# Kernel optimization log

Measured on AMD Instinct MI355X. Metric: run time of the kernel, lower is better.

The kernel has to match this reference:

```python
import jax, jax.numpy as jnp
import numpy as np

S, B, D, NH = 4096, 4, 1024, 16


def _unitnorm(v):
    # v / ||v||_2 along last dim (matches torch.norm(v, dim=-1))
    return v / jnp.linalg.norm(v, axis=-1, keepdims=True)


def setup_inputs() -> dict:
    key = jax.random.key(0)
    ks = jax.random.split(key, 9)
    scale = 1.0 / np.sqrt(D)
    inp = {
        "h": jax.random.normal(ks[0], (S, B, D), dtype=jnp.float32),
        "Wq_w": jax.random.normal(ks[1], (D, D), dtype=jnp.float32) * scale,
        "Wq_b": jax.random.normal(ks[2], (D,), dtype=jnp.float32) * scale,
        "Wk_w": jax.random.normal(ks[3], (D, D), dtype=jnp.float32) * scale,
        "Wk_b": jax.random.normal(ks[4], (D,), dtype=jnp.float32) * scale,
        "Wv_w": jax.random.normal(ks[5], (D, D), dtype=jnp.float32) * scale,
        "Wv_b": jax.random.normal(ks[6], (D,), dtype=jnp.float32) * scale,
        "Wo_w": jax.random.normal(ks[7], (D, D), dtype=jnp.float32) * scale,
        "Wo_b": jax.random.normal(ks[8], (D,), dtype=jnp.float32) * scale,
        "nhead": NH,
    }
    return inp


def reference(h, Wq_w, Wq_b, Wk_w, Wk_b, Wv_w, Wv_b, Wo_w, Wo_b, nhead):
    s, b, d = h.shape
    dh = d // nhead

    def proj(W, bias):
        # torch nn.Linear: x @ W.T + b, then split heads -> [S,B,NH,dh]
        return (h @ W.T + bias).reshape(s, b, nhead, dh)

    k = jax.nn.elu(_unitnorm(proj(Wk_w, Wk_b)))  # unitelu
    v = proj(Wv_w, Wv_b)
    q = _unitnorm(proj(Wq_w, Wq_b))  # sigma = unitnorm (default)

    # Linear-attention state: sum of outer products over the whole sequence
    A = jnp.einsum('sbnq,sbnv->bnvq', k, v)  # [B,NH,dh,dh]
    out = jnp.einsum('sbnq,bnvq->sbnv', q, A).reshape(s, b, d)
    out = out @ Wo_w.T + Wo_b
    return out, k, q
```

## Files before the change

### kernel.cpp

```cpp
#include <hip/hip_runtime.h>
#include <hip/hip_bf16.h>
#include <math.h>

#define S_LEN 4096
#define B_SZ  4
#define D_DIM 1024
#define NHEAD 16
#define R_ROWS (S_LEN * B_SZ)

#define AS1 __attribute__((address_space(1)))
#define AS3 __attribute__((address_space(3)))

typedef __bf16 bf16_t;
typedef __attribute__((ext_vector_type(8))) __bf16 bf16x8;
typedef __attribute__((ext_vector_type(4))) __bf16 bf16x4;
typedef __attribute__((ext_vector_type(4))) float  f32x4;

#define MFMA16 __builtin_amdgcn_mfma_f32_16x16x32_bf16

__device__ __forceinline__ void gload16(const bf16_t* g, bf16_t* l) {
  __builtin_amdgcn_global_load_lds((const AS1 unsigned int*)g,
                                   (AS3 unsigned int*)l, 16, 0, 0);
}

#define BAR asm volatile("s_barrier" ::: "memory")
#define LGKM0 do { asm volatile("s_waitcnt lgkmcnt(0)" ::: "memory"); \
                   __builtin_amdgcn_sched_barrier(0); } while (0)

#define RD_A(dst, ap, mlo) \
  _Pragma("unroll") for (int mm = 0; mm < 4; ++mm) \
    _Pragma("unroll") for (int kx = 0; kx < 2; ++kx) \
      dst[mm][kx] = *(const bf16x8*)&ap[offA[(mlo) + mm][kx]];
#define RD_B(dst, bp, nlo) \
  _Pragma("unroll") for (int nn = 0; nn < 2; ++nn) \
    _Pragma("unroll") for (int kx = 0; kx < 2; ++kx) \
      dst[nn][kx] = *(const bf16x8*)&bp[offB[(nlo) + nn][kx]];
#define QUAD(mb, nb, AF, BF) \
  do { __builtin_amdgcn_s_setprio(1); \
  _Pragma("unroll") for (int kx = 0; kx < 2; ++kx) \
    _Pragma("unroll") for (int mm = 0; mm < 4; ++mm) \
      _Pragma("unroll") for (int nn = 0; nn < 2; ++nn) \
        acc[(mb)+mm][(nb)+nn] = MFMA16(AF[mm][kx], BF[nn][kx], acc[(mb)+mm][(nb)+nn], 0, 0, 0); \
  __builtin_amdgcn_s_setprio(0); } while (0)

__global__ void k_cvt(const float* __restrict__ src, bf16_t* __restrict__ dst, int n) {
  int i = (blockIdx.x * 256 + threadIdx.x) * 4;
  if (i >= n) return;
  f32x4 v = *(const f32x4*)(src + i);
  bf16x4 o;
  o[0] = (bf16_t)v[0]; o[1] = (bf16_t)v[1]; o[2] = (bf16_t)v[2]; o[3] = (bf16_t)v[3];
  *(bf16x4*)(dst + i) = o;
}
__global__ void k_cvtw(const float* __restrict__ q, const float* __restrict__ k,
                       const float* __restrict__ v, const float* __restrict__ o,
                       bf16_t* __restrict__ dst) {
  const int sec = blockIdx.x >> 10;
  const int i = ((blockIdx.x & 1023) * 256 + threadIdx.x) * 4;
  const float* s = (sec == 0) ? q : (sec == 1) ? k : (sec == 2) ? v : o;
  f32x4 x = *(const f32x4*)(s + i);
  bf16x4 y;
  y[0] = (bf16_t)x[0]; y[1] = (bf16_t)x[1]; y[2] = (bf16_t)x[2]; y[3] = (bf16_t)x[3];
  *(bf16x4*)(dst + (size_t)sec * 1048576 + i) = y;
}

__device__ __forceinline__ void gemm_core_8ph(
    const bf16_t* __restrict__ A, const bf16_t* __restrict__ B,
    int row0, int col0,
    bf16_t (&sA)[2][2][8192], bf16_t (&sB)[2][2][8192], f32x4 (&acc)[8][4])
{
  const int tid  = threadIdx.x;
  const int wave = tid >> 6, lane = tid & 63;
  const int lr = lane & 15, lg = lane >> 4;
  const int wr = wave >> 2, wn = wave & 3;
  const int grow = tid >> 3;
  const int gsw  = (tid & 7) ^ (grow & 7);

  auto stA = [&](int buf, int half, int k0) {
    #pragma unroll
    for (int j = 0; j < 2; ++j)
      gload16(&A[(size_t)(row0 + half * 128 + j * 64 + grow) * D_DIM + k0 + gsw * 8],
              &sA[buf][half][(j * 64 + wave * 8) * 64]);
  };
  auto stB = [&](int buf, int half, int k0) {
    #pragma unroll
    for (int j = 0; j < 2; ++j)
      gload16(&B[(size_t)(col0 + half * 128 + j * 64 + grow) * D_DIM + k0 + gsw * 8],
              &sB[buf][half][(j * 64 + wave * 8) * 64]);
  };

  int offA[8][2], offB[4][2];
  #pragma unroll
  for (int m = 0; m < 8; ++m) {
    const int r = m * 16 + lr;
    #pragma unroll
    for (int kx = 0; kx < 2; ++kx)
      offA[m][kx] = r * 64 + (((kx << 2) + lg) ^ (r & 7)) * 8;
  }
  #pragma unroll
  for (int n = 0; n < 4; ++n) {
    const int r = (wn & 1) * 64 + n * 16 + lr;
    #pragma unroll
    for (int kx = 0; kx < 2; ++kx)
      offB[n][kx] = r * 64 + (((kx << 2) + lg) ^ (r & 7)) * 8;
  }
  const bf16_t* a0 = &sA[0][wr][0];
  const bf16_t* a1 = &sA[1][wr][0];
  const bf16_t* b0 = &sB[0][wn >> 1][0];
  const bf16_t* b1 = &sB[1][wn >> 1][0];

  #pragma unroll
  for (int m = 0; m < 8; m++)
    #pragma unroll
    for (int n = 0; n < 4; n++)
      #pragma unroll
      for (int r = 0; r < 4; r++) acc[m][n][r] = 0.f;

  stA(0, 0, 0);  stA(0, 1, 0);  stB(0, 0, 0);  stB(0, 1, 0);
  stA(1, 0, 64); stA(1, 1, 64); stB(1, 0, 64); stB(1, 1, 64);
  asm volatile("s_waitcnt vmcnt(8)" ::: "memory");
  BAR;

  bf16x8 af03[4][2], af47[4][2], bf01[2][2], bf23[2][2];

  #pragma unroll 1
  for (int i = 0; i < 8; ++i) {
    const bool last = (i == 7);
    const int kn0 = (i + 1) * 128, kn1 = kn0 + 64;

    RD_A(af03, a0, 0); RD_B(bf01, b0, 0);
    LGKM0; QUAD(0, 0, af03, bf01); BAR;
    RD_A(af47, a0, 4);
    LGKM0; QUAD(4, 0, af47, bf01); BAR;
    RD_B(bf23, b0, 2);
    if (!last) stA(0, 0, kn0);
    LGKM0; QUAD(0, 2, af03, bf23); BAR;
    if (!last) { stA(0, 1, kn0); stB(0, 0, kn0); }
    QUAD(4, 2, af47, bf23);
    if (!last) asm volatile("s_waitcnt vmcnt(6)" ::: "memory");
    else       asm volatile("s_waitcnt vmcnt(0)" ::: "memory");
    BAR;

    RD_A(af03, a1, 0); RD_B(bf01, b1, 0);
    if (!last) stB(0, 1, kn0);
    LGKM0; QUAD(0, 0, af03, bf01); BAR;
    RD_A(af47, a1, 4);
    LGKM0; QUAD(4, 0, af47, bf01); BAR;
    RD_B(bf23, b1, 2);
    if (!last) stA(1, 0, kn1);
    LGKM0; QUAD(0, 2, af03, bf23); BAR;
    if (!last) { stA(1, 1, kn1); stB(1, 0, kn1); stB(1, 1, kn1); }
    QUAD(4, 2, af47, bf23);
    if (!last) asm volatile("s_waitcnt vmcnt(8)" ::: "memory");
    BAR;
  }
}

__global__ __launch_bounds__(512, 2) void k_proj(
    const bf16_t* __restrict__ hB, const bf16_t* __restrict__ Wcat,
    const float* __restrict__ bq, const float* __restrict__ bk, const float* __restrict__ bv,
    bf16_t* __restrict__ outVb, float* __restrict__ outK, float* __restrict__ outQ,
    bf16_t* __restrict__ qBm)
{
  __shared__ bf16_t sA[2][2][8192];
  __shared__ bf16_t sB[2][2][8192];

  const int tid  = threadIdx.x;
  const int wave = tid >> 6, lane = tid & 63;
  const int lr = lane & 15, lg = lane >> 4;
  const int wr = wave >> 2, wn = wave & 3;
  const int row0 = blockIdx.x * 256;
  const int by   = blockIdx.y;

  f32x4 acc[8][4];
  gemm_core_8ph(hB, Wcat, row0, by * 256, sA, sB, acc);

  const int sec = by >> 2;
  const int hc0 = (by & 3) * 256 + wn * 64;
  const float* bias = (sec == 0) ? bq : (sec == 1 ? bk : bv);
  float bvv[4];
  #pragma unroll
  for (int n = 0; n < 4; n++) bvv[n] = bias[hc0 + n * 16 + lr];

  #pragma unroll
  for (int m = 0; m < 8; ++m) {
    #pragma unroll
    for (int r = 0; r < 4; ++r) {
      const int gm = row0 + wr * 128 + m * 16 + lg * 4 + r;
      float v[4];
      float ss = 0.f;
      #pragma unroll
      for (int n = 0; n < 4; n++) {
        v[n] = acc[m][n][r] + bvv[n];
        ss += v[n] * v[n];
      }
      if (sec == 2) {
        #pragma unroll
        for (int n = 0; n < 4; n++)
          outVb[(size_t)gm * D_DIM + hc0 + n * 16 + lr] = (bf16_t)v[n];
      } else {
        #pragma unroll
        for (int msk = 1; msk < 16; msk <<= 1) ss += __shfl_xor(ss, msk);
        const float rs = 1.0f / sqrtf(ss);
        if (sec == 0) {
          const size_t qrow = (size_t)(gm & 3) * S_LEN + (gm >> 2);
          #pragma unroll
          for (int n = 0; n < 4; n++) {
            const float qn = v[n] * rs;
            outQ[(size_t)gm * D_DIM + hc0 + n * 16 + lr] = qn;
            qBm[qrow * D_DIM + hc0 + n * 16 + lr] = (bf16_t)qn;
          }
        } else {
          #pragma unroll
          for (int n = 0; n < 4; n++) {
            float kn = v[n] * rs;
            kn = kn > 0.f ? kn : expm1f(kn);
            outK[(size_t)gm * D_DIM + hc0 + n * 16 + lr] = kn;
          }
        }
      }
    }
  }
}

__global__ __launch_bounds__(256) void k_state(
    const float* __restrict__ Kf, const bf16_t* __restrict__ Vb,
    float* __restrict__ Apart)
{
  const int bn = blockIdx.x;
  const int ch = blockIdx.y;
  const int b = bn >> 4, n = bn & 15;
  const int tid = threadIdx.x;
  const int ti = tid >> 4, tj = tid & 15;

  __shared__ float sV[32][64];
  __shared__ float sK[32][64];

  float acc[4][4];
  #pragma unroll
  for (int i = 0; i < 4; i++)
    #pragma unroll
    for (int j = 0; j < 4; j++) acc[i][j] = 0.f;

  const int rr = tid >> 3, cc = (tid & 7) * 8;
  for (int s0 = ch * 512; s0 < ch * 512 + 512; s0 += 32) {
    const size_t g = (size_t)((s0 + rr) * B_SZ + b) * D_DIM + n * 64 + cc;
    bf16x8 v8 = *(const bf16x8*)&Vb[g];
    #pragma unroll
    for (int e = 0; e < 8; e++) sV[rr][cc + e] = (float)v8[e];
    *(f32x4*)&sK[rr][cc]     = *(const f32x4*)&Kf[g];
    *(f32x4*)&sK[rr][cc + 4] = *(const f32x4*)&Kf[g + 4];
    __syncthreads();
    #pragma unroll
    for (int ss = 0; ss < 32; ss++) {
      f32x4 vv = *(const f32x4*)&sV[ss][ti * 4];
      f32x4 kk = *(const f32x4*)&sK[ss][tj * 4];
      #pragma unroll
      for (int i = 0; i < 4; i++)
        #pragma unroll
        for (int j = 0; j < 4; j++)
          acc[i][j] = fmaf(vv[i], kk[j], acc[i][j]);
    }
    __syncthreads();
  }
  float* ap = Apart + ((size_t)ch * 64 + bn) * 4096;
  #pragma unroll
  for (int i = 0; i < 4; i++)
    #pragma unroll
    for (int j = 0; j < 4; j++)
      ap[(ti * 4 + i) * 64 + tj * 4 + j] = acc[i][j];
}

__global__ __launch_bounds__(256) void k_combine(
    const float* __restrict__ Apart, const bf16_t* __restrict__ WoB,
    bf16_t* __restrict__ Ct)
{
  const int bn = blockIdx.x;
  const int dp = blockIdx.y;
  const int b = bn >> 4, n = bn & 15;
  const int tid = threadIdx.x;
  const int ti = tid >> 4, tj = tid & 15;

  __shared__ float sAm[64][65];
  __shared__ float sW[64][65];

  #pragma unroll
  for (int p = 0; p < 16; p++) {
    const int idx = tid + p * 256;
    float s = 0.f;
    #pragma unroll
    for (int c2 = 0; c2 < 8; c2++)
      s += Apart[((size_t)c2 * 64 + bn) * 4096 + idx];
    sAm[idx >> 6][idx & 63] = s;
  }
  {
    const int r = tid >> 2, cv = (tid & 3) * 16;
    bf16x8 w0 = *(const bf16x8*)&WoB[(size_t)(dp * 64 + r) * D_DIM + n * 64 + cv];
    bf16x8 w1 = *(const bf16x8*)&WoB[(size_t)(dp * 64 + r) * D_DIM + n * 64 + cv + 8];
    #pragma unroll
    for (int e = 0; e < 8; e++) {
      sW[r][cv + e]     = (float)w0[e];
      sW[r][cv + 8 + e] = (float)w1[e];
    }
  }
  __syncthreads();

  float acc[4][4];
  #pragma unroll
  for (int i = 0; i < 4; i++)
    #pragma unroll
    for (int j = 0; j < 4; j++) acc[i][j] = 0.f;

  for (int dv = 0; dv < 64; dv++) {
    float w[4], a[4];
    #pragma unroll
    for (int i = 0; i < 4; i++) w[i] = sW[ti * 4 + i][dv];
    #pragma unroll
    for (int j = 0; j < 4; j++) a[j] = sAm[dv][tj * 4 + j];
    #pragma unroll
    for (int i = 0; i < 4; i++)
      #pragma unroll
      for (int j = 0; j < 4; j++)
        acc[i][j] = fmaf(w[i], a[j], acc[i][j]);
  }
  #pragma unroll
  for (int i = 0; i < 4; i++)
    #pragma unroll
    for (int j = 0; j < 4; j++)
      Ct[((size_t)b * D_DIM + dp * 64 + ti * 4 + i) * D_DIM + n * 64 + tj * 4 + j] =
          (bf16_t)acc[i][j];
}

__global__ __launch_bounds__(512, 2) void k_final(
    const bf16_t* __restrict__ qBm, const bf16_t* __restrict__ Ct,
    const float* __restrict__ bo, float* __restrict__ outO)
{
  __shared__ bf16_t sA[2][2][8192];
  __shared__ bf16_t sB[2][2][8192];

  const int tid  = threadIdx.x;
  const int wave = tid >> 6, lane = tid & 63;
  const int lr = lane & 15, lg = lane >> 4;
  const int wr = wave >> 2, wn = wave & 3;
  const int b    = blockIdx.z;
  const int row0 = blockIdx.x * 256;
  const int col0 = blockIdx.y * 256;

  f32x4 acc[8][4];
  gemm_core_8ph(qBm + (size_t)b * S_LEN * D_DIM, Ct + (size_t)b * D_DIM * D_DIM,
                row0, col0, sA, sB, acc);

  #pragma unroll
  for (int m = 0; m < 8; ++m) {
    #pragma unroll
    for (int r = 0; r < 4; ++r) {
      const int gs = row0 + wr * 128 + m * 16 + lg * 4 + r;
      #pragma unroll
      for (int n = 0; n < 4; n++) {
        const int col = col0 + wn * 64 + n * 16 + lr;
        outO[((size_t)gs * B_SZ + b) * D_DIM + col] = acc[m][n][r] + bo[col];
      }
    }
  }
}

extern "C" void kernel_launch(void* const* d_in, const int* in_sizes, int n_in,
                              void* d_out, int out_size, void* d_ws, size_t ws_size,
                              hipStream_t stream) {
  (void)in_sizes; (void)n_in; (void)out_size; (void)ws_size;
  const float* h  = (const float*)d_in[0];
  const float* Wq = (const float*)d_in[1];
  const float* bq = (const float*)d_in[2];
  const float* Wk = (const float*)d_in[3];
  const float* bk = (const float*)d_in[4];
  const float* Wv = (const float*)d_in[5];
  const float* bv = (const float*)d_in[6];
  const float* Wo = (const float*)d_in[7];
  const float* bo = (const float*)d_in[8];

  float* out0 = (float*)d_out;
  float* outK = out0 + (size_t)R_ROWS * D_DIM;
  float* outQ = outK + (size_t)R_ROWS * D_DIM;
  bf16_t* vB  = (bf16_t*)d_out;

  char* ws = (char*)d_ws;
  bf16_t* hB    = (bf16_t*)ws;
  bf16_t* Ct    = (bf16_t*)ws;
  bf16_t* Wcat  = (bf16_t*)(ws + 33554432);
  bf16_t* WoB   = (bf16_t*)(ws + 33554432 + 6291456);
  float*  Apart = (float*)(ws + 41943040);
  bf16_t* qBm   = (bf16_t*)(ws + 50331648);

  const int nH = R_ROWS * D_DIM;
  k_cvt<<<nH / 1024, 256, 0, stream>>>(h, hB, nH);
  k_cvtw<<<4096, 256, 0, stream>>>(Wq, Wk, Wv, Wo, Wcat);

  k_proj<<<dim3(64, 12), 512, 0, stream>>>(hB, Wcat, bq, bk, bv,
                                           vB, outK, outQ, qBm);
  k_state<<<dim3(64, 8), 256, 0, stream>>>(outK, vB, Apart);
  k_combine<<<dim3(64, 16), 256, 0, stream>>>(Apart, WoB, Ct);
  k_final<<<dim3(S_LEN / 256, D_DIM / 256, B_SZ), 512, 0, stream>>>(qBm, Ct, bo, out0);
}
```

Measured before the change: 243.5 us.

## Switch GEMM cores to 32x32x16 MFMA with new LDS swizzle and staging

Replaces the 16x16x32 bf16 MFMA tiling in the shared GEMM core with 32x32x16 MFMA. Each wave now holds 4x2 tiles of 16-float accumulators, and the LDS read addressing and XOR swizzle change to match the 32-row fragment layout. The per-half-buffer global-to-LDS staging is regrouped into a single burst after the third phase. The epilogues of the projection and final kernels are rewritten for the 32x32 output layout, with the row-norm shuffle now spanning 32 lanes. The aim is fewer MFMA issues and fewer LDS reads per FLOP. The trade-off is a changed load/compute overlap schedule and possible register pressure.

```diff
diff --git a/kernel.cpp b/kernel.cpp
--- a/kernel.cpp
+++ b/kernel.cpp
@@ -15,8 +15,9 @@
 typedef __attribute__((ext_vector_type(8))) __bf16 bf16x8;
 typedef __attribute__((ext_vector_type(4))) __bf16 bf16x4;
 typedef __attribute__((ext_vector_type(4))) float  f32x4;
-
-#define MFMA16 __builtin_amdgcn_mfma_f32_16x16x32_bf16
+typedef __attribute__((ext_vector_type(16))) float f32x16;
+
+#define MFMA32 __builtin_amdgcn_mfma_f32_32x32x16_bf16
 
 __device__ __forceinline__ void gload16(const bf16_t* g, bf16_t* l) {
   __builtin_amdgcn_global_load_lds((const AS1 unsigned int*)g,
@@ -27,20 +28,20 @@
 #define LGKM0 do { asm volatile("s_waitcnt lgkmcnt(0)" ::: "memory"); \
                    __builtin_amdgcn_sched_barrier(0); } while (0)
 
-#define RD_A(dst, ap, mlo) \
+#define RDA(dst, ap, ksp) \
   _Pragma("unroll") for (int mm = 0; mm < 4; ++mm) \
-    _Pragma("unroll") for (int kx = 0; kx < 2; ++kx) \
-      dst[mm][kx] = *(const bf16x8*)&ap[offA[(mlo) + mm][kx]];
-#define RD_B(dst, bp, nlo) \
+    _Pragma("unroll") for (int j = 0; j < 2; ++j) \
+      dst[mm][j] = *(const bf16x8*)&ap[rA64[mm] + ((((4*(ksp) + 2*j) + hl) ^ gA[mm]) << 3)];
+#define RDB(dst, bp, ksp) \
   _Pragma("unroll") for (int nn = 0; nn < 2; ++nn) \
-    _Pragma("unroll") for (int kx = 0; kx < 2; ++kx) \
-      dst[nn][kx] = *(const bf16x8*)&bp[offB[(nlo) + nn][kx]];
-#define QUAD(mb, nb, AF, BF) \
+    _Pragma("unroll") for (int j = 0; j < 2; ++j) \
+      dst[nn][j] = *(const bf16x8*)&bp[rB64[nn] + ((((4*(ksp) + 2*j) + hl) ^ gB[nn]) << 3)];
+#define OCT(mb, AF, BF) \
   do { __builtin_amdgcn_s_setprio(1); \
-  _Pragma("unroll") for (int kx = 0; kx < 2; ++kx) \
-    _Pragma("unroll") for (int mm = 0; mm < 4; ++mm) \
+  _Pragma("unroll") for (int j = 0; j < 2; ++j) \
+    _Pragma("unroll") for (int mm = 0; mm < 2; ++mm) \
       _Pragma("unroll") for (int nn = 0; nn < 2; ++nn) \
-        acc[(mb)+mm][(nb)+nn] = MFMA16(AF[mm][kx], BF[nn][kx], acc[(mb)+mm][(nb)+nn], 0, 0, 0); \
+        acc[(mb)+mm][nn] = MFMA32(AF[(mb)+mm][j], BF[nn][j], acc[(mb)+mm][nn], 0, 0, 0); \
   __builtin_amdgcn_s_setprio(0); } while (0)
 
 __global__ void k_cvt(const float* __restrict__ src, bf16_t* __restrict__ dst, int n) {
@@ -63,17 +64,17 @@
   *(bf16x4*)(dst + (size_t)sec * 1048576 + i) = y;
 }
 
-__device__ __forceinline__ void gemm_core_8ph(
+__device__ __forceinline__ void gemm_core_32(
     const bf16_t* __restrict__ A, const bf16_t* __restrict__ B,
     int row0, int col0,
-    bf16_t (&sA)[2][2][8192], bf16_t (&sB)[2][2][8192], f32x4 (&acc)[8][4])
+    bf16_t (&sA)[2][2][8192], bf16_t (&sB)[2][2][8192], f32x16 (&acc)[4][2])
 {
   const int tid  = threadIdx.x;
   const int wave = tid >> 6, lane = tid & 63;
-  const int lr = lane & 15, lg = lane >> 4;
+  const int l31 = lane & 31, hl = lane >> 5;
   const int wr = wave >> 2, wn = wave & 3;
   const int grow = tid >> 3;
-  const int gsw  = (tid & 7) ^ (grow & 7);
+  const int gsw  = (tid & 7) ^ (grow & 7) ^ ((grow >> 3) & 3);
 
   auto stA = [&](int buf, int half, int k0) {
     #pragma unroll
@@ -88,68 +89,63 @@
               &sB[buf][half][(j * 64 + wave * 8) * 64]);
   };
 
-  int offA[8][2], offB[4][2];
-  #pragma unroll
-  for (int m = 0; m < 8; ++m) {
-    const int r = m * 16 + lr;
-    #pragma unroll
-    for (int kx = 0; kx < 2; ++kx)
-      offA[m][kx] = r * 64 + (((kx << 2) + lg) ^ (r & 7)) * 8;
-  }
-  #pragma unroll
-  for (int n = 0; n < 4; ++n) {
-    const int r = (wn & 1) * 64 + n * 16 + lr;
-    #pragma unroll
-    for (int kx = 0; kx < 2; ++kx)
-      offB[n][kx] = r * 64 + (((kx << 2) + lg) ^ (r & 7)) * 8;
-  }
-  const bf16_t* a0 = &sA[0][wr][0];
-  const bf16_t* a1 = &sA[1][wr][0];
-  const bf16_t* b0 = &sB[0][wn >> 1][0];
-  const bf16_t* b1 = &sB[1][wn >> 1][0];
-
-  #pragma unroll
-  for (int m = 0; m < 8; m++)
-    #pragma unroll
-    for (int n = 0; n < 4; n++)
+  int rA64[4], gA[4], rB64[2], gB[2];
+  #pragma unroll
+  for (int m = 0; m < 4; ++m) {
+    const int r = m * 32 + l31;
+    rA64[m] = r * 64;
+    gA[m]   = (r & 7) ^ ((r >> 3) & 3);
+  }
+  #pragma unroll
+  for (int n = 0; n < 2; ++n) {
+    const int r = (wn & 1) * 64 + n * 32 + l31;
+    rB64[n] = r * 64;
+    gB[n]   = (r & 7) ^ ((r >> 3) & 3);
+  }
+  const bf16_t* aH0 = &sA[0][wr][0];
+  const bf16_t* aH1 = &sA[1][wr][0];
+  const bf16_t* bH0 = &sB[0][wn >> 1][0];
+  const bf16_t* bH1 = &sB[1][wn >> 1][0];
+
+  #pragma unroll
+  for (int m = 0; m < 4; m++)
+    #pragma unroll
+    for (int n = 0; n < 2; n++)
       #pragma unroll
-      for (int r = 0; r < 4; r++) acc[m][n][r] = 0.f;
+      for (int r = 0; r < 16; r++) acc[m][n][r] = 0.f;
 
   stA(0, 0, 0);  stA(0, 1, 0);  stB(0, 0, 0);  stB(0, 1, 0);
   stA(1, 0, 64); stA(1, 1, 64); stB(1, 0, 64); stB(1, 1, 64);
   asm volatile("s_waitcnt vmcnt(8)" ::: "memory");
   BAR;
 
-  bf16x8 af03[4][2], af47[4][2], bf01[2][2], bf23[2][2];
+  bf16x8 afL[4][2], afH[4][2], bfL[2][2], bfH[2][2];
 
   #pragma unroll 1
   for (int i = 0; i < 8; ++i) {
     const bool last = (i == 7);
     const int kn0 = (i + 1) * 128, kn1 = kn0 + 64;
 
-    RD_A(af03, a0, 0); RD_B(bf01, b0, 0);
-    LGKM0; QUAD(0, 0, af03, bf01); BAR;
-    RD_A(af47, a0, 4);
-    LGKM0; QUAD(4, 0, af47, bf01); BAR;
-    RD_B(bf23, b0, 2);
-    if (!last) stA(0, 0, kn0);
-    LGKM0; QUAD(0, 2, af03, bf23); BAR;
-    if (!last) { stA(0, 1, kn0); stB(0, 0, kn0); }
-    QUAD(4, 2, af47, bf23);
-    if (!last) asm volatile("s_waitcnt vmcnt(6)" ::: "memory");
+    RDA(afL, aH0, 0); RDB(bfL, bH0, 0);
+    LGKM0; OCT(0, afL, bfL); BAR;
+    RDA(afH, aH0, 1);
+    OCT(2, afL, bfL); BAR;
+    RDB(bfH, bH0, 1);
+    LGKM0; OCT(0, afH, bfH); BAR;
+    if (!last) { stA(0, 0, kn0); stA(0, 1, kn0); stB(0, 0, kn0); stB(0, 1, kn0); }
+    OCT(2, afH, bfH);
+    if (!last) asm volatile("s_waitcnt vmcnt(8)" ::: "memory");
     else       asm volatile("s_waitcnt vmcnt(0)" ::: "memory");
     BAR;
 
-    RD_A(af03, a1, 0); RD_B(bf01, b1, 0);
-    if (!last) stB(0, 1, kn0);
-    LGKM0; QUAD(0, 0, af03, bf01); BAR;
-    RD_A(af47, a1, 4);
-    LGKM0; QUAD(4, 0, af47, bf01); BAR;
-    RD_B(bf23, b1, 2);
-    if (!last) stA(1, 0, kn1);
-    LGKM0; QUAD(0, 2, af03, bf23); BAR;
-    if (!last) { stA(1, 1, kn1); stB(1, 0, kn1); stB(1, 1, kn1); }
-    QUAD(4, 2, af47, bf23);
+    RDA(afL, aH1, 0); RDB(bfL, bH1, 0);
+    LGKM0; OCT(0, afL, bfL); BAR;
+    RDA(afH, aH1, 1);
+    OCT(2, afL, bfL); BAR;
+    RDB(bfH, bH1, 1);
+    LGKM0; OCT(0, afH, bfH); BAR;
+    if (!last) { stA(1, 0, kn1); stA(1, 1, kn1); stB(1, 0, kn1); stB(1, 1, kn1); }
+    OCT(2, afH, bfH);
     if (!last) asm volatile("s_waitcnt vmcnt(8)" ::: "memory");
     BAR;
   }
@@ -166,56 +162,48 @@
 
   const int tid  = threadIdx.x;
   const int wave = tid >> 6, lane = tid & 63;
-  const int lr = lane & 15, lg = lane >> 4;
+  const int l31 = lane & 31, hl = lane >> 5;
   const int wr = wave >> 2, wn = wave & 3;
   const int row0 = blockIdx.x * 256;
   const int by   = blockIdx.y;
 
-  f32x4 acc[8][4];
-  gemm_core_8ph(hB, Wcat, row0, by * 256, sA, sB, acc);
+  f32x16 acc[4][2];
+  gemm_core_32(hB, Wcat, row0, by * 256, sA, sB, acc);
 
   const int sec = by >> 2;
   const int hc0 = (by & 3) * 256 + wn * 64;
   const float* bias = (sec == 0) ? bq : (sec == 1 ? bk : bv);
-  float bvv[4];
-  #pragma unroll
-  for (int n = 0; n < 4; n++) bvv[n] = bias[hc0 + n * 16 + lr];
-
-  #pragma unroll
-  for (int m = 0; m < 8; ++m) {
-    #pragma unroll
-    for (int r = 0; r < 4; ++r) {
-      const int gm = row0 + wr * 128 + m * 16 + lg * 4 + r;
-      float v[4];
-      float ss = 0.f;
-      #pragma unroll
-      for (int n = 0; n < 4; n++) {
-        v[n] = acc[m][n][r] + bvv[n];
-        ss += v[n] * v[n];
-      }
+  const float bv0 = bias[hc0 + l31];
+  const float bv1 = bias[hc0 + 32 + l31];
+
+  #pragma unroll
+  for (int m = 0; m < 4; ++m) {
+    #pragma unroll
+    for (int reg = 0; reg < 16; ++reg) {
+      const int gm = row0 + wr * 128 + m * 32 + (reg & 3) + 8 * (reg >> 2) + 4 * hl;
+      float v0 = acc[m][0][reg] + bv0;
+      float v1 = acc[m][1][reg] + bv1;
       if (sec == 2) {
+        outVb[(size_t)gm * D_DIM + hc0 + l31]      = (bf16_t)v0;
+        outVb[(size_t)gm * D_DIM + hc0 + 32 + l31] = (bf16_t)v1;
+      } else {
+        float ss = v0 * v0 + v1 * v1;
         #pragma unroll
-        for (int n = 0; n < 4; n++)
-          outVb[(size_t)gm * D_DIM + hc0 + n * 16 + lr] = (bf16_t)v[n];
-      } else {
-        #pragma unroll
-        for (int msk = 1; msk < 16; msk <<= 1) ss += __shfl_xor(ss, msk);
+        for (int msk = 1; msk < 32; msk <<= 1) ss += __shfl_xor(ss, msk);
         const float rs = 1.0f / sqrtf(ss);
         if (sec == 0) {
           const size_t qrow = (size_t)(gm & 3) * S_LEN + (gm >> 2);
-          #pragma unroll
-          for (int n = 0; n < 4; n++) {
-            const float qn = v[n] * rs;
-            outQ[(size_t)gm * D_DIM + hc0 + n * 16 + lr] = qn;
-            qBm[qrow * D_DIM + hc0 + n * 16 + lr] = (bf16_t)qn;
-          }
+          const float q0 = v0 * rs, q1 = v1 * rs;
+          outQ[(size_t)gm * D_DIM + hc0 + l31]      = q0;
+          outQ[(size_t)gm * D_DIM + hc0 + 32 + l31] = q1;
+          qBm[qrow * D_DIM + hc0 + l31]      = (bf16_t)q0;
+          qBm[qrow * D_DIM + hc0 + 32 + l31] = (bf16_t)q1;
         } else {
-          #pragma unroll
-          for (int n = 0; n < 4; n++) {
-            float kn = v[n] * rs;
-            kn = kn > 0.f ? kn : expm1f(kn);
-            outK[(size_t)gm * D_DIM + hc0 + n * 16 + lr] = kn;
-          }
+          float k0 = v0 * rs, k1 = v1 * rs;
+          k0 = k0 > 0.f ? k0 : expm1f(k0);
+          k1 = k1 > 0.f ? k1 : expm1f(k1);
+          outK[(size_t)gm * D_DIM + hc0 + l31]      = k0;
+          outK[(size_t)gm * D_DIM + hc0 + 32 + l31] = k1;
         }
       }
     }
@@ -339,26 +327,26 @@
 
   const int tid  = threadIdx.x;
   const int wave = tid >> 6, lane = tid & 63;
-  const int lr = lane & 15, lg = lane >> 4;
+  const int l31 = lane & 31, hl = lane >> 5;
   const int wr = wave >> 2, wn = wave & 3;
   const int b    = blockIdx.z;
   const int row0 = blockIdx.x * 256;
   const int col0 = blockIdx.y * 256;
 
-  f32x4 acc[8][4];
-  gemm_core_8ph(qBm + (size_t)b * S_LEN * D_DIM, Ct + (size_t)b * D_DIM * D_DIM,
-                row0, col0, sA, sB, acc);
-
-  #pragma unroll
-  for (int m = 0; m < 8; ++m) {
-    #pragma unroll
-    for (int r = 0; r < 4; ++r) {
-      const int gs = row0 + wr * 128 + m * 16 + lg * 4 + r;
-      #pragma unroll
-      for (int n = 0; n < 4; n++) {
-        const int col = col0 + wn * 64 + n * 16 + lr;
-        outO[((size_t)gs * B_SZ + b) * D_DIM + col] = acc[m][n][r] + bo[col];
-      }
+  f32x16 acc[4][2];
+  gemm_core_32(qBm + (size_t)b * S_LEN * D_DIM, Ct + (size_t)b * D_DIM * D_DIM,
+               row0, col0, sA, sB, acc);
+
+  const int cb = col0 + wn * 64;
+  const float bo0 = bo[cb + l31];
+  const float bo1 = bo[cb + 32 + l31];
+  #pragma unroll
+  for (int m = 0; m < 4; ++m) {
+    #pragma unroll
+    for (int reg = 0; reg < 16; ++reg) {
+      const int gs = row0 + wr * 128 + m * 32 + (reg & 3) + 8 * (reg >> 2) + 4 * hl;
+      outO[((size_t)gs * B_SZ + b) * D_DIM + cb + l31]      = acc[m][0][reg] + bo0;
+      outO[((size_t)gs * B_SZ + b) * D_DIM + cb + 32 + l31] = acc[m][1][reg] + bo1;
     }
   }
 }
```

Result: slower. 290.4 us (+19.3%).
